# Optimization experiments

Hardware: AMD Instinct MI355X
Metric: run time of the kernel (lower is better)

The kernel has to match this reference:

```python
import jax, jax.numpy as jnp
import numpy as np

B, D, U, HU = 2048, 1024, 1024, 256

def _ln(x, eps=1e-3):
    # Keras LayerNormalization(center=False, scale=False), default epsilon=1e-3
    m = jnp.mean(x, axis=-1, keepdims=True)
    v = jnp.var(x, axis=-1, keepdims=True)
    return (x - m) * jax.lax.rsqrt(v + eps)

def setup_inputs() -> dict:
    key = jax.random.key(0)
    ks = jax.random.split(key, 17)
    s = 0.02
    return {
        "inputs": jax.random.normal(ks[0], (B, D), jnp.float32),
        "main_h": 0.1 * jax.random.normal(ks[1], (B, U), jnp.float32),
        "main_c": 0.1 * jax.random.normal(ks[2], (B, U), jnp.float32),
        "hyper_h": 0.1 * jax.random.normal(ks[3], (B, HU), jnp.float32),
        "hyper_c": 0.1 * jax.random.normal(ks[4], (B, HU), jnp.float32),
        "kernel": s * jax.random.normal(ks[5], (D, 4 * U), jnp.float32),
        "recurrent_kernel": s * jax.random.normal(ks[6], (U, 4 * U), jnp.float32),
        "bias": jnp.zeros((4 * U,), jnp.float32),
        "hyper_kernel": s * jax.random.normal(ks[7], (D + U, 4 * HU), jnp.float32),
        "hyper_rec_kernel": s * jax.random.normal(ks[8], (HU, 4 * HU), jnp.float32),
        "hyper_bias": jnp.zeros((4 * HU,), jnp.float32),
        "dx_w": s * jax.random.normal(ks[9], (HU, 4 * U), jnp.float32),
        "dx_b": s * jax.random.normal(ks[10], (4 * U,), jnp.float32),
        "dh_w": s * jax.random.normal(ks[11], (HU, 4 * U), jnp.float32),
        "dh_b": s * jax.random.normal(ks[12], (4 * U,), jnp.float32),
        "db_w": s * jax.random.normal(ks[13], (HU, 4 * U), jnp.float32),
        "db_b": s * jax.random.normal(ks[14], (4 * U,), jnp.float32),
    }

def reference(inputs, main_h, main_c, hyper_h, hyper_c,
              kernel, recurrent_kernel, bias,
              hyper_kernel, hyper_rec_kernel, hyper_bias,
              dx_w, dx_b, dh_w, dh_b, db_w, db_b):
    # --- hyper LSTMCell (Keras gate order i, f, g, o) ---
    hx = jnp.concatenate([inputs, main_h], axis=-1)          # [B, D+U]
    z = hx @ hyper_kernel + hyper_h @ hyper_rec_kernel + hyper_bias  # [B, 4*HU]
    hi, hf, hg, ho = jnp.split(z, 4, axis=-1)
    hyper_c_new = jax.nn.sigmoid(hf) * hyper_c + jax.nn.sigmoid(hi) * jnp.tanh(hg)
    hyper_out = jax.nn.sigmoid(ho) * jnp.tanh(hyper_c_new)  # = hyper_h_new

    # --- hypernet gate scalings ---
    d_x = hyper_out @ dx_w + dx_b                            # [B, 4*U]
    d_h = hyper_out @ dh_w + dh_b
    d_b = hyper_out @ db_w + db_b

    # --- main LSTM gates with hyper modulation + LayerNorm ---
    proj_x = inputs @ kernel + bias                          # [B, 4*U]
    proj_h = main_h @ recurrent_kernel                       # [B, 4*U]
    gates = _ln(d_x * proj_x + d_h * proj_h + d_b)
    i, f, g, o = jnp.split(gates, 4, axis=-1)
    main_c_new = jax.nn.sigmoid(f) * main_c + jax.nn.sigmoid(i) * jnp.tanh(g)
    main_h_new = jax.nn.sigmoid(o) * jnp.tanh(_ln(main_c_new))
    return (main_h_new, main_c_new, hyper_out, hyper_c_new)
```

## Files before the change

### kernel.cpp

```cpp
#include <hip/hip_runtime.h>
#include <cstdint>

typedef unsigned short u16;
typedef _Float16 half8 __attribute__((ext_vector_type(8)));
typedef float floatx4 __attribute__((ext_vector_type(4)));

#define BB 2048
#define UU 1024
#define HUx 256
#define O_H  0
#define O_C  (BB*UU)
#define O_HO (2*BB*UU)
#define O_HC (2*BB*UU + BB*HUx)
#define MFMAH __builtin_amdgcn_mfma_f32_16x16x32_f16

#define LBAR() do { \
    asm volatile("s_waitcnt lgkmcnt(0)\n\ts_barrier" ::: "memory"); \
    __builtin_amdgcn_sched_barrier(0); \
} while (0)

__device__ __forceinline__ float bf2f(u16 u) {
    union { uint32_t i; float f; } v; v.i = ((uint32_t)u) << 16; return v.f;
}
__device__ __forceinline__ u16 f2bf(float f) {
    union { float f; uint32_t i; } v; v.f = f;
    uint32_t r = v.i + 0x7fffu + ((v.i >> 16) & 1u);
    return (u16)(r >> 16);
}
__device__ __forceinline__ u16 f2h(float f) {
    _Float16 h = (_Float16)f; u16 u; __builtin_memcpy(&u, &h, 2); return u;
}
__device__ __forceinline__ float sigf(float x) { return 1.f / (1.f + expf(-x)); }
__device__ __forceinline__ float ldmix(const void* p, size_t i, int isbf) {
    return isbf ? bf2f(((const u16*)p)[i]) : ((const float*)p)[i];
}
__device__ __forceinline__ u16 ld2h(const void* p, size_t i, int isbf) {
    return f2h(ldmix(p, i, isbf));
}

__device__ __forceinline__ void stage_sync(u16* lds, const u16* src, int row0, int ldK,
                                           int k0, int rows, int tid) {
    for (int v = tid; v < rows * 4; v += 256) {
        int r = v >> 2, c = (v & 3) * 8;
        half8 d = *(const half8*)(src + (size_t)(row0 + r) * ldK + k0 + c);
        *(half8*)&lds[r * 40 + c] = d;
    }
}

__device__ __forceinline__ void ld128(half8 r[2], const u16* src, int row0, int ldK,
                                      int k0, int tid) {
    #pragma unroll
    for (int i = 0; i < 2; i++) {
        int v = tid + 256 * i;
        r[i] = *(const half8*)(src + (size_t)(row0 + (v >> 2)) * ldK + k0 + (v & 3) * 8);
    }
}
__device__ __forceinline__ void ld64(half8& r, const u16* src, int row0, int ldK,
                                     int k0, int tid) {
    r = *(const half8*)(src + (size_t)(row0 + (tid >> 2)) * ldK + k0 + (tid & 3) * 8);
}
__device__ __forceinline__ void wr128(u16* lds, const half8 r[2], int tid) {
    #pragma unroll
    for (int i = 0; i < 2; i++) {
        int v = tid + 256 * i;
        *(half8*)&lds[(v >> 2) * 40 + (v & 3) * 8] = r[i];
    }
}
__device__ __forceinline__ void wr64(u16* lds, half8 r, int tid) {
    *(half8*)&lds[(tid >> 2) * 40 + (tid & 3) * 8] = r;
}

__global__ void detect_dtype(const u16* __restrict__ raw, int* __restrict__ flag) {
    u16 u = raw[2 * threadIdx.x];
    int e = (u >> 7) & 0xFF;
    unsigned long long m = __ballot(e >= 100 && e <= 134);
    if (threadIdx.x == 0) *flag = (__popcll(m) >= 32) ? 1 : 0;
}

__global__ void cvt_all(const void* __restrict__ xs, const void* __restrict__ ms,
                        const void* __restrict__ hs, u16* __restrict__ xh,
                        u16* __restrict__ mh, u16* __restrict__ hh, const int* __restrict__ flag) {
    int i = blockIdx.x * 256 + threadIdx.x;
    int isbf = *flag;
    const void* src; u16* dst; int t;
    if (i < 262144)      { src = xs; dst = xh; t = i; }
    else if (i < 524288) { src = ms; dst = mh; t = i - 262144; }
    else                 { src = hs; dst = hh; t = i - 524288; }
    #pragma unroll
    for (int j = 0; j < 8; j++)
        dst[(size_t)t * 8 + j] = ld2h(src, (size_t)t * 8 + j, isbf);
}

__global__ void transpose_cvt(const void* __restrict__ in, u16* __restrict__ out,
                              int R, int C, int ostride, int ocol,
                              const int* __restrict__ flag) {
    __shared__ u16 th[32][33];
    int isbf = *flag;
    int c0 = blockIdx.x * 32, r0 = blockIdx.y * 32;
    int tx = threadIdx.x, ty = threadIdx.y;
    #pragma unroll
    for (int i = 0; i < 32; i += 8)
        th[ty + i][tx] = ld2h(in, (size_t)(r0 + ty + i) * C + c0 + tx, isbf);
    __syncthreads();
    #pragma unroll
    for (int i = 0; i < 32; i += 8)
        out[(size_t)(c0 + ty + i) * ostride + ocol + r0 + tx] = th[tx][ty + i];
}

__global__ void transpose_z(const void* __restrict__ i0, const void* __restrict__ i1,
                            const void* __restrict__ i2, u16* __restrict__ o0,
                            u16* __restrict__ o1, u16* __restrict__ o2,
                            int R, int C, int ostride, const int* __restrict__ flag) {
    __shared__ u16 th[32][33];
    const void* in = (blockIdx.z == 0) ? i0 : (blockIdx.z == 1) ? i1 : i2;
    u16* out = (blockIdx.z == 0) ? o0 : (blockIdx.z == 1) ? o1 : o2;
    int isbf = *flag;
    int c0 = blockIdx.x * 32, r0 = blockIdx.y * 32;
    int tx = threadIdx.x, ty = threadIdx.y;
    #pragma unroll
    for (int i = 0; i < 32; i += 8)
        th[ty + i][tx] = ld2h(in, (size_t)(r0 + ty + i) * C + c0 + tx, isbf);
    __syncthreads();
    #pragma unroll
    for (int i = 0; i < 32; i += 8)
        out[(size_t)(c0 + ty + i) * ostride + r0 + tx] = th[tx][ty + i];
}

__device__ __forceinline__ void gh_load(half8 pA[2], half8& pB,
                                        const u16* xh, const u16* mh, const u16* hh,
                                        const u16* BT, int bm, int bn, int s, int tid) {
    const u16* Ap; int ldA, kA;
    if (s < 32)      { Ap = xh; ldA = 1024; kA = s * 32; }
    else if (s < 64) { Ap = mh; ldA = 1024; kA = (s - 32) * 32; }
    else             { Ap = hh; ldA = 256;  kA = (s - 64) * 32; }
    ld128(pA, Ap, bm, ldA, kA, tid);
    ld64(pB, BT, bn, 2304, s * 32, tid);
}

__global__ __launch_bounds__(256) void gemm_hyper(const u16* __restrict__ xh,
                                                  const u16* __restrict__ mh,
                                                  const u16* __restrict__ hh,
                                                  const u16* __restrict__ BT,
                                                  float* __restrict__ z) {
    __shared__ __align__(16) u16 sA[128 * 40];
    __shared__ __align__(16) u16 sB[64 * 40];
    int tid = threadIdx.x, lane = tid & 63, wave = tid >> 6;
    int wm = (wave & 1) * 64, wn = (wave >> 1) * 32;
    int bm = blockIdx.y * 128, bn = blockIdx.x * 64;
    int s0 = blockIdx.z * 36, s1 = s0 + 36;
    floatx4 acc[4][2] = {};
    int mr = lane & 15, kq = (lane >> 4) * 8;

    half8 pA[2]; half8 pB;
    gh_load(pA, pB, xh, mh, hh, BT, bm, bn, s0, tid);
    wr128(sA, pA, tid); wr64(sB, pB, tid);
    gh_load(pA, pB, xh, mh, hh, BT, bm, bn, s0 + 1, tid);
    LBAR();

    #pragma unroll 1
    for (int s = s0; s < s1; s++) {
        half8 a[4], b[2];
        #pragma unroll
        for (int t = 0; t < 4; t++) a[t] = *(const half8*)&sA[(wm + t * 16 + mr) * 40 + kq];
        #pragma unroll
        for (int t = 0; t < 2; t++) b[t] = *(const half8*)&sB[(wn + t * 16 + mr) * 40 + kq];
        #pragma unroll
        for (int tm = 0; tm < 4; tm++)
            #pragma unroll
            for (int tn = 0; tn < 2; tn++)
                acc[tm][tn] = MFMAH(a[tm], b[tn], acc[tm][tn], 0, 0, 0);
        LBAR();
        if (s < s1 - 1) {
            wr128(sA, pA, tid); wr64(sB, pB, tid);
            if (s < s1 - 2)
                gh_load(pA, pB, xh, mh, hh, BT, bm, bn, s + 2, tid);
            LBAR();
        }
    }

    float* zp = z + (size_t)blockIdx.z * 2048 * 1024;
    #pragma unroll
    for (int tm = 0; tm < 4; tm++)
        #pragma unroll
        for (int tn = 0; tn < 2; tn++) {
            int col = bn + wn + tn * 16 + (lane & 15);
            #pragma unroll
            for (int rr = 0; rr < 4; rr++) {
                int row = bm + wm + tm * 16 + (lane >> 4) * 4 + rr;
                zp[(size_t)row * 1024 + col] = acc[tm][tn][rr];
            }
        }
}

__global__ void hyper_cell(const float* __restrict__ z, const void* __restrict__ hyper_c,
                           const void* __restrict__ hyper_bias, void* __restrict__ out,
                           u16* __restrict__ ho16, const int* __restrict__ flag) {
    int isbf = *flag;
    int t = blockIdx.x * 256 + threadIdx.x;
    int k = t & 255;
    const float* zr  = z + (size_t)(t >> 8) * 1024;
    const float* zr2 = zr + (size_t)2048 * 1024;
    float hi = zr[k]       + zr2[k]       + ldmix(hyper_bias, k, isbf);
    float hf = zr[k + 256] + zr2[k + 256] + ldmix(hyper_bias, k + 256, isbf);
    float hg = zr[k + 512] + zr2[k + 512] + ldmix(hyper_bias, k + 512, isbf);
    float ho = zr[k + 768] + zr2[k + 768] + ldmix(hyper_bias, k + 768, isbf);
    float c  = ldmix(hyper_c, t, isbf);
    float cn = sigf(hf) * c + sigf(hi) * tanhf(hg);
    float hout = sigf(ho) * tanhf(cn);
    ho16[t] = f2h(hout);
    if (isbf) {
        ((u16*)out)[O_HO + t] = f2bf(hout);
        ((u16*)out)[O_HC + t] = f2bf(cn);
    } else {
        ((float*)out)[O_HO + t] = hout;
        ((float*)out)[O_HC + t] = cn;
    }
}

__global__ __launch_bounds__(256, 2) void mega_fused(
    const u16* __restrict__ xh, const u16* __restrict__ mh, const u16* __restrict__ ho16,
    const u16* __restrict__ kT, const u16* __restrict__ rkT,
    const u16* __restrict__ dxT, const u16* __restrict__ dhT, const u16* __restrict__ dbT,
    const void* __restrict__ bias, const void* __restrict__ dx_b,
    const void* __restrict__ dh_b, const void* __restrict__ db_b,
    u16* __restrict__ gp, const int* __restrict__ flag) {
    __shared__ __align__(16) u16 sA1[128 * 40];
    __shared__ __align__(16) u16 sA2[128 * 40];
    __shared__ __align__(16) u16 sB1[64 * 40];
    __shared__ __align__(16) u16 sB2[64 * 40];
    __shared__ __align__(16) u16 sB3[64 * 40];
    int isbf = *flag;
    int tid = threadIdx.x, lane = tid & 63, wave = tid >> 6;
    int wm = (wave & 1) * 64, wn = (wave >> 1) * 32;
    int bm = blockIdx.y * 128, bn = blockIdx.x * 64;
    floatx4 apx[4][2] = {}, aph[4][2] = {}, adx[4][2] = {}, adh[4][2] = {}, adb[4][2] = {};
    int mr = lane & 15, kq = (lane >> 4) * 8;

    half8 nA1[2], nA2[2], nB1a, nB2a, nB3a;

    ld128(nA1, xh,  bm, 1024, 0, tid);
    ld128(nA2, mh,  bm, 1024, 0, tid);
    ld64(nB1a, kT,  bn, 1024, 0, tid);
    ld64(nB2a, rkT, bn, 1024, 0, tid);
    wr128(sA1, nA1, tid); wr128(sA2, nA2, tid);
    wr64(sB1, nB1a, tid); wr64(sB2, nB2a, tid);
    ld128(nA1, xh,  bm, 1024, 32, tid);
    ld128(nA2, mh,  bm, 1024, 32, tid);
    ld64(nB1a, kT,  bn, 1024, 32, tid);
    ld64(nB2a, rkT, bn, 1024, 32, tid);
    LBAR();

    #pragma unroll 1
    for (int k0 = 0; k0 < 1024; k0 += 32) {
        half8 ax[4], am[4], bk[2], br[2];
        #pragma unroll
        for (int t = 0; t < 4; t++) {
            int ra = (wm + t * 16 + mr) * 40 + kq;
            ax[t] = *(const half8*)&sA1[ra];
            am[t] = *(const half8*)&sA2[ra];
        }
        #pragma unroll
        for (int t = 0; t < 2; t++) {
            int rb = (wn + t * 16 + mr) * 40 + kq;
            bk[t] = *(const half8*)&sB1[rb];
            br[t] = *(const half8*)&sB2[rb];
        }
        #pragma unroll
        for (int tm = 0; tm < 4; tm++)
            #pragma unroll
            for (int tn = 0; tn < 2; tn++) {
                apx[tm][tn] = MFMAH(ax[tm], bk[tn], apx[tm][tn], 0, 0, 0);
                aph[tm][tn] = MFMAH(am[tm], br[tn], aph[tm][tn], 0, 0, 0);
            }
        LBAR();
        if (k0 < 1024 - 32) {
            wr128(sA1, nA1, tid); wr128(sA2, nA2, tid);
            wr64(sB1, nB1a, tid); wr64(sB2, nB2a, tid);
            if (k0 < 1024 - 64) {
                ld128(nA1, xh,  bm, 1024, k0 + 64, tid);
                ld128(nA2, mh,  bm, 1024, k0 + 64, tid);
                ld64(nB1a, kT,  bn, 1024, k0 + 64, tid);
                ld64(nB2a, rkT, bn, 1024, k0 + 64, tid);
            } else {
                ld128(nA1, ho16, bm, 256, 0, tid);
                ld64(nB1a, dxT,  bn, 256, 0, tid);
                ld64(nB2a, dhT,  bn, 256, 0, tid);
                ld64(nB3a, dbT,  bn, 256, 0, tid);
            }
            LBAR();
        }
    }

    wr128(sA1, nA1, tid);
    wr64(sB1, nB1a, tid); wr64(sB2, nB2a, tid); wr64(sB3, nB3a, tid);
    ld128(nA1, ho16, bm, 256, 32, tid);
    ld64(nB1a, dxT,  bn, 256, 32, tid);
    ld64(nB2a, dhT,  bn, 256, 32, tid);
    ld64(nB3a, dbT,  bn, 256, 32, tid);
    LBAR();

    #pragma unroll 1
    for (int k0 = 0; k0 < 256; k0 += 32) {
        half8 a[4], bx[2], bh[2], bb[2];
        #pragma unroll
        for (int t = 0; t < 4; t++) {
            int ra = (wm + t * 16 + mr) * 40 + kq;
            a[t] = *(const half8*)&sA1[ra];
        }
        #pragma unroll
        for (int t = 0; t < 2; t++) {
            int rb = (wn + t * 16 + mr) * 40 + kq;
            bx[t] = *(const half8*)&sB1[rb];
            bh[t] = *(const half8*)&sB2[rb];
            bb[t] = *(const half8*)&sB3[rb];
        }
        #pragma unroll
        for (int tm = 0; tm < 4; tm++)
            #pragma unroll
            for (int tn = 0; tn < 2; tn++) {
                adx[tm][tn] = MFMAH(a[tm], bx[tn], adx[tm][tn], 0, 0, 0);
                adh[tm][tn] = MFMAH(a[tm], bh[tn], adh[tm][tn], 0, 0, 0);
                adb[tm][tn] = MFMAH(a[tm], bb[tn], adb[tm][tn], 0, 0, 0);
            }
        LBAR();
        if (k0 < 256 - 32) {
            wr128(sA1, nA1, tid);
            wr64(sB1, nB1a, tid); wr64(sB2, nB2a, tid); wr64(sB3, nB3a, tid);
            if (k0 < 256 - 64) {
                ld128(nA1, ho16, bm, 256, k0 + 64, tid);
                ld64(nB1a, dxT,  bn, 256, k0 + 64, tid);
                ld64(nB2a, dhT,  bn, 256, k0 + 64, tid);
                ld64(nB3a, dbT,  bn, 256, k0 + 64, tid);
            }
            LBAR();
        }
    }

    #pragma unroll
    for (int tn = 0; tn < 2; tn++) {
        int col = bn + wn + tn * 16 + (lane & 15);
        float bv  = ldmix(bias, col, isbf);
        float dxb = ldmix(dx_b, col, isbf);
        float dhb = ldmix(dh_b, col, isbf);
        float dbb = ldmix(db_b, col, isbf);
        #pragma unroll
        for (int tm = 0; tm < 4; tm++) {
            #pragma unroll
            for (int rr = 0; rr < 4; rr++) {
                int row = bm + wm + tm * 16 + (lane >> 4) * 4 + rr;
                float px = apx[tm][tn][rr] + bv;
                float ph = aph[tm][tn][rr];
                float dx = adx[tm][tn][rr] + dxb;
                float dh = adh[tm][tn][rr] + dhb;
                float db = adb[tm][tn][rr] + dbb;
                gp[(size_t)row * 4096 + col] = f2h(dx * px + dh * ph + db);
            }
        }
    }
}

__device__ __forceinline__ void block_reduce2(float& a, float& b, float* red) {
    #pragma unroll
    for (int o = 32; o > 0; o >>= 1) {
        a += __shfl_down(a, o, 64);
        b += __shfl_down(b, o, 64);
    }
    int lane = threadIdx.x & 63, w = threadIdx.x >> 6;
    if (lane == 0) { red[w] = a; red[4 + w] = b; }
    __syncthreads();
    a = red[0] + red[1] + red[2] + red[3];
    b = red[4] + red[5] + red[6] + red[7];
    __syncthreads();
}

__global__ __launch_bounds__(256) void ln_main(const u16* __restrict__ gp,
                                               const void* __restrict__ main_c,
                                               void* __restrict__ out,
                                               const int* __restrict__ flag) {
    __shared__ float sPre[4096];
    __shared__ float sC[1024];
    __shared__ float red[8];
    int isbf = *flag;
    int b = blockIdx.x, tid = threadIdx.x;
    const u16* g = gp + (size_t)b * 4096;
    float s = 0.f, q = 0.f;
    for (int j0 = tid * 8; j0 < 4096; j0 += 2048) {
        half8 v = *(const half8*)(g + j0);
        #pragma unroll
        for (int e = 0; e < 8; e++) {
            float f = (float)v[e];
            sPre[j0 + e] = f; s += f; q += f * f;
        }
    }
    block_reduce2(s, q, red);
    float mean = s * (1.f / 4096.f);
    float var = q * (1.f / 4096.f) - mean * mean;
    float rs = rsqrtf(var + 1e-3f);
    float s2 = 0.f, q2 = 0.f;
    for (int u = tid; u < 1024; u += 256) {
        float gi = (sPre[u] - mean) * rs;
        float gf = (sPre[u + 1024] - mean) * rs;
        float gg = (sPre[u + 2048] - mean) * rs;
        float c = ldmix(main_c, (size_t)b * 1024 + u, isbf);
        float cn = sigf(gf) * c + sigf(gi) * tanhf(gg);
        sC[u] = cn;
        if (isbf) ((u16*)out)[O_C + (size_t)b * 1024 + u] = f2bf(cn);
        else      ((float*)out)[O_C + (size_t)b * 1024 + u] = cn;
        s2 += cn; q2 += cn * cn;
    }
    block_reduce2(s2, q2, red);
    float m2 = s2 * (1.f / 1024.f);
    float v2 = q2 * (1.f / 1024.f) - m2 * m2;
    float rs2 = rsqrtf(v2 + 1e-3f);
    for (int u = tid; u < 1024; u += 256) {
        float go = (sPre[u + 3072] - mean) * rs;
        float hn = sigf(go) * tanhf((sC[u] - m2) * rs2);
        if (isbf) ((u16*)out)[O_H + (size_t)b * 1024 + u] = f2bf(hn);
        else      ((float*)out)[O_H + (size_t)b * 1024 + u] = hn;
    }
}

extern "C" void kernel_launch(void* const* d_in, const int* in_sizes, int n_in,
                              void* d_out, int out_size, void* d_ws, size_t ws_size,
                              hipStream_t stream) {
    (void)in_sizes; (void)n_in; (void)out_size; (void)ws_size;
    const void* inputs   = d_in[0];
    const void* main_h   = d_in[1];
    const void* main_c   = d_in[2];
    const void* hyper_h  = d_in[3];
    const void* hyper_c  = d_in[4];
    const void* kernel_w = d_in[5];
    const void* rec_w    = d_in[6];
    const void* bias     = d_in[7];
    const void* hyper_k  = d_in[8];
    const void* hyper_rk = d_in[9];
    const void* hyper_b  = d_in[10];
    const void* dx_w = d_in[11];
    const void* dx_b = d_in[12];
    const void* dh_w = d_in[13];
    const void* dh_b = d_in[14];
    const void* db_w = d_in[15];
    const void* db_b = d_in[16];
    char* ws = (char*)d_ws;
    const size_t MB = 1024 * 1024;

    int* flag = (int*)ws;
    size_t off = 256;
    u16* xh  = (u16*)(ws + off); off += 4 * MB;
    u16* mh  = (u16*)(ws + off); off += 4 * MB;
    u16* hh  = (u16*)(ws + off); off += 1 * MB;
    u16* ho  = (u16*)(ws + off); off += 1 * MB;
    u16* kT  = (u16*)(ws + off); off += 8 * MB;
    u16* rkT = (u16*)(ws + off); off += 8 * MB;
    u16* dxT = (u16*)(ws + off); off += 2 * MB;
    u16* dhT = (u16*)(ws + off); off += 2 * MB;
    u16* dbT = (u16*)(ws + off); off += 2 * MB;
    u16* BTh = (u16*)(ws + off); off += (size_t)1024 * 2304 * 2;
    float* zbuf = (float*)(ws + off); off += 16 * MB;
    u16* gp    = (u16*)(ws + off); off += 16 * MB;

    detect_dtype<<<1, 64, 0, stream>>>((const u16*)inputs, flag);
    cvt_all<<<2304, 256, 0, stream>>>(inputs, main_h, hyper_h, xh, mh, hh, flag);

    dim3 tblk(32, 8);
    transpose_cvt<<<dim3(32, 64), tblk, 0, stream>>>(hyper_k, BTh, 2048, 1024, 2304, 0, flag);
    transpose_cvt<<<dim3(32, 8),  tblk, 0, stream>>>(hyper_rk, BTh, 256, 1024, 2304, 2048, flag);
    transpose_z<<<dim3(128, 32, 2), tblk, 0, stream>>>(kernel_w, rec_w, rec_w,
                                                       kT, rkT, rkT, 1024, 4096, 1024, flag);
    transpose_z<<<dim3(128, 8, 3), tblk, 0, stream>>>(dx_w, dh_w, db_w,
                                                      dxT, dhT, dbT, 256, 4096, 256, flag);

    gemm_hyper<<<dim3(16, 16, 2), 256, 0, stream>>>(xh, mh, hh, BTh, zbuf);
    hyper_cell<<<2048, 256, 0, stream>>>(zbuf, hyper_c, hyper_b, d_out, ho, flag);
    mega_fused<<<dim3(64, 16), 256, 0, stream>>>(xh, mh, ho, kT, rkT, dxT, dhT, dbT,
                                                 bias, dx_b, dh_b, db_b, gp, flag);
    ln_main<<<2048, 256, 0, stream>>>(gp, main_c, d_out, flag);
}
```

Before: 299.4 us.

## Load A operands directly from global into registers, bypassing LDS

The A-matrix tiles (inputs, main_h, hyper_out) are now loaded by each wave straight from global memory into MFMA operand registers, double-buffered across unrolled K steps, instead of being staged through shared memory. This removes the LDS write/read traffic and LDS space for A, which may allow more occupancy. In exchange, A rows are re-fetched from global/L2 by both N-direction waves, and the per-lane 16-byte loads are less coalesced. Register pressure also rises from holding four extra half8 sets.

```diff
diff --git a/kernel.cpp b/kernel.cpp
--- a/kernel.cpp
+++ b/kernel.cpp
@@ -38,15 +38,6 @@
     return f2h(ldmix(p, i, isbf));
 }
 
-__device__ __forceinline__ void stage_sync(u16* lds, const u16* src, int row0, int ldK,
-                                           int k0, int rows, int tid) {
-    for (int v = tid; v < rows * 4; v += 256) {
-        int r = v >> 2, c = (v & 3) * 8;
-        half8 d = *(const half8*)(src + (size_t)(row0 + r) * ldK + k0 + c);
-        *(half8*)&lds[r * 40 + c] = d;
-    }
-}
-
 __device__ __forceinline__ void ld128(half8 r[2], const u16* src, int row0, int ldK,
                                       int k0, int tid) {
     #pragma unroll
@@ -68,6 +59,13 @@
 }
 __device__ __forceinline__ void wr64(u16* lds, half8 r, int tid) {
     *(half8*)&lds[(tid >> 2) * 40 + (tid & 3) * 8] = r;
+}
+
+__device__ __forceinline__ void ldA4(half8 r[4], const u16* src, int row0, int ldK,
+                                     int k0, int mr, int kq) {
+    #pragma unroll
+    for (int t = 0; t < 4; t++)
+        r[t] = *(const half8*)(src + (size_t)(row0 + t * 16 + mr) * ldK + k0 + kq);
 }
 
 __global__ void detect_dtype(const u16* __restrict__ raw, int* __restrict__ flag) {
@@ -224,8 +222,6 @@
     const void* __restrict__ bias, const void* __restrict__ dx_b,
     const void* __restrict__ dh_b, const void* __restrict__ db_b,
     u16* __restrict__ gp, const int* __restrict__ flag) {
-    __shared__ __align__(16) u16 sA1[128 * 40];
-    __shared__ __align__(16) u16 sA2[128 * 40];
     __shared__ __align__(16) u16 sB1[64 * 40];
     __shared__ __align__(16) u16 sB2[64 * 40];
     __shared__ __align__(16) u16 sB3[64 * 40];
@@ -235,106 +231,106 @@
     int bm = blockIdx.y * 128, bn = blockIdx.x * 64;
     floatx4 apx[4][2] = {}, aph[4][2] = {}, adx[4][2] = {}, adh[4][2] = {}, adb[4][2] = {};
     int mr = lane & 15, kq = (lane >> 4) * 8;
-
-    half8 nA1[2], nA2[2], nB1a, nB2a, nB3a;
-
-    ld128(nA1, xh,  bm, 1024, 0, tid);
-    ld128(nA2, mh,  bm, 1024, 0, tid);
+    int arow = bm + wm;
+
+    half8 nB1a, nB2a, nB3a;
+    half8 axA[4], amA[4], axB[4], amB[4];
+
     ld64(nB1a, kT,  bn, 1024, 0, tid);
     ld64(nB2a, rkT, bn, 1024, 0, tid);
-    wr128(sA1, nA1, tid); wr128(sA2, nA2, tid);
     wr64(sB1, nB1a, tid); wr64(sB2, nB2a, tid);
-    ld128(nA1, xh,  bm, 1024, 32, tid);
-    ld128(nA2, mh,  bm, 1024, 32, tid);
     ld64(nB1a, kT,  bn, 1024, 32, tid);
     ld64(nB2a, rkT, bn, 1024, 32, tid);
+    ldA4(axA, xh, arow, 1024, 0, mr, kq);
+    ldA4(amA, mh, arow, 1024, 0, mr, kq);
     LBAR();
 
+    #define P1_STEP(AXC, AMC, AXN, AMN, K0)                                    \
+    do {                                                                       \
+        if ((K0) + 32 < 1024) {                                                \
+            ldA4(AXN, xh, arow, 1024, (K0) + 32, mr, kq);                      \
+            ldA4(AMN, mh, arow, 1024, (K0) + 32, mr, kq);                      \
+        }                                                                      \
+        half8 bk[2], br[2];                                                    \
+        _Pragma("unroll")                                                      \
+        for (int t = 0; t < 2; t++) {                                          \
+            int rb = (wn + t * 16 + mr) * 40 + kq;                             \
+            bk[t] = *(const half8*)&sB1[rb];                                   \
+            br[t] = *(const half8*)&sB2[rb];                                   \
+        }                                                                      \
+        _Pragma("unroll")                                                      \
+        for (int tm = 0; tm < 4; tm++)                                         \
+            _Pragma("unroll")                                                  \
+            for (int tn = 0; tn < 2; tn++) {                                   \
+                apx[tm][tn] = MFMAH((AXC)[tm], bk[tn], apx[tm][tn], 0, 0, 0);  \
+                aph[tm][tn] = MFMAH((AMC)[tm], br[tn], aph[tm][tn], 0, 0, 0);  \
+            }                                                                  \
+        LBAR();                                                                \
+        if ((K0) < 992) {                                                      \
+            wr64(sB1, nB1a, tid); wr64(sB2, nB2a, tid);                        \
+            if ((K0) < 960) {                                                  \
+                ld64(nB1a, kT,  bn, 1024, (K0) + 64, tid);                     \
+                ld64(nB2a, rkT, bn, 1024, (K0) + 64, tid);                     \
+            } else {                                                           \
+                ld64(nB1a, dxT, bn, 256, 0, tid);                              \
+                ld64(nB2a, dhT, bn, 256, 0, tid);                              \
+                ld64(nB3a, dbT, bn, 256, 0, tid);                              \
+            }                                                                  \
+            LBAR();                                                            \
+        }                                                                      \
+    } while (0)
+
     #pragma unroll 1
-    for (int k0 = 0; k0 < 1024; k0 += 32) {
-        half8 ax[4], am[4], bk[2], br[2];
-        #pragma unroll
-        for (int t = 0; t < 4; t++) {
-            int ra = (wm + t * 16 + mr) * 40 + kq;
-            ax[t] = *(const half8*)&sA1[ra];
-            am[t] = *(const half8*)&sA2[ra];
-        }
-        #pragma unroll
-        for (int t = 0; t < 2; t++) {
-            int rb = (wn + t * 16 + mr) * 40 + kq;
-            bk[t] = *(const half8*)&sB1[rb];
-            br[t] = *(const half8*)&sB2[rb];
-        }
-        #pragma unroll
-        for (int tm = 0; tm < 4; tm++)
-            #pragma unroll
-            for (int tn = 0; tn < 2; tn++) {
-                apx[tm][tn] = MFMAH(ax[tm], bk[tn], apx[tm][tn], 0, 0, 0);
-                aph[tm][tn] = MFMAH(am[tm], br[tn], aph[tm][tn], 0, 0, 0);
-            }
-        LBAR();
-        if (k0 < 1024 - 32) {
-            wr128(sA1, nA1, tid); wr128(sA2, nA2, tid);
-            wr64(sB1, nB1a, tid); wr64(sB2, nB2a, tid);
-            if (k0 < 1024 - 64) {
-                ld128(nA1, xh,  bm, 1024, k0 + 64, tid);
-                ld128(nA2, mh,  bm, 1024, k0 + 64, tid);
-                ld64(nB1a, kT,  bn, 1024, k0 + 64, tid);
-                ld64(nB2a, rkT, bn, 1024, k0 + 64, tid);
-            } else {
-                ld128(nA1, ho16, bm, 256, 0, tid);
-                ld64(nB1a, dxT,  bn, 256, 0, tid);
-                ld64(nB2a, dhT,  bn, 256, 0, tid);
-                ld64(nB3a, dbT,  bn, 256, 0, tid);
-            }
-            LBAR();
-        }
-    }
-
-    wr128(sA1, nA1, tid);
+    for (int k0 = 0; k0 < 1024; k0 += 64) {
+        P1_STEP(axA, amA, axB, amB, k0);
+        P1_STEP(axB, amB, axA, amA, k0 + 32);
+    }
+    #undef P1_STEP
+
     wr64(sB1, nB1a, tid); wr64(sB2, nB2a, tid); wr64(sB3, nB3a, tid);
-    ld128(nA1, ho16, bm, 256, 32, tid);
-    ld64(nB1a, dxT,  bn, 256, 32, tid);
-    ld64(nB2a, dhT,  bn, 256, 32, tid);
-    ld64(nB3a, dbT,  bn, 256, 32, tid);
+    ld64(nB1a, dxT, bn, 256, 32, tid);
+    ld64(nB2a, dhT, bn, 256, 32, tid);
+    ld64(nB3a, dbT, bn, 256, 32, tid);
+    ldA4(axA, ho16, arow, 256, 0, mr, kq);
     LBAR();
 
+    #define P2_STEP(AC, AN, K0)                                                \
+    do {                                                                       \
+        if ((K0) + 32 < 256) ldA4(AN, ho16, arow, 256, (K0) + 32, mr, kq);     \
+        half8 bx[2], bh[2], bb[2];                                             \
+        _Pragma("unroll")                                                      \
+        for (int t = 0; t < 2; t++) {                                          \
+            int rb = (wn + t * 16 + mr) * 40 + kq;                             \
+            bx[t] = *(const half8*)&sB1[rb];                                   \
+            bh[t] = *(const half8*)&sB2[rb];                                   \
+            bb[t] = *(const half8*)&sB3[rb];                                   \
+        }                                                                      \
+        _Pragma("unroll")                                                      \
+        for (int tm = 0; tm < 4; tm++)                                         \
+            _Pragma("unroll")                                                  \
+            for (int tn = 0; tn < 2; tn++) {                                   \
+                adx[tm][tn] = MFMAH((AC)[tm], bx[tn], adx[tm][tn], 0, 0, 0);   \
+                adh[tm][tn] = MFMAH((AC)[tm], bh[tn], adh[tm][tn], 0, 0, 0);   \
+                adb[tm][tn] = MFMAH((AC)[tm], bb[tn], adb[tm][tn], 0, 0, 0);   \
+            }                                                                  \
+        LBAR();                                                                \
+        if ((K0) < 224) {                                                      \
+            wr64(sB1, nB1a, tid); wr64(sB2, nB2a, tid); wr64(sB3, nB3a, tid);  \
+            if ((K0) < 192) {                                                  \
+                ld64(nB1a, dxT, bn, 256, (K0) + 64, tid);                      \
+                ld64(nB2a, dhT, bn, 256, (K0) + 64, tid);                      \
+                ld64(nB3a, dbT, bn, 256, (K0) + 64, tid);                      \
+            }                                                                  \
+            LBAR();                                                            \
+        }                                                                      \
+    } while (0)
+
     #pragma unroll 1
-    for (int k0 = 0; k0 < 256; k0 += 32) {
-        half8 a[4], bx[2], bh[2], bb[2];
-        #pragma unroll
-        for (int t = 0; t < 4; t++) {
-            int ra = (wm + t * 16 + mr) * 40 + kq;
-            a[t] = *(const half8*)&sA1[ra];
-        }
-        #pragma unroll
-        for (int t = 0; t < 2; t++) {
-            int rb = (wn + t * 16 + mr) * 40 + kq;
-            bx[t] = *(const half8*)&sB1[rb];
-            bh[t] = *(const half8*)&sB2[rb];
-            bb[t] = *(const half8*)&sB3[rb];
-        }
-        #pragma unroll
-        for (int tm = 0; tm < 4; tm++)
-            #pragma unroll
-            for (int tn = 0; tn < 2; tn++) {
-                adx[tm][tn] = MFMAH(a[tm], bx[tn], adx[tm][tn], 0, 0, 0);
-                adh[tm][tn] = MFMAH(a[tm], bh[tn], adh[tm][tn], 0, 0, 0);
-                adb[tm][tn] = MFMAH(a[tm], bb[tn], adb[tm][tn], 0, 0, 0);
-            }
-        LBAR();
-        if (k0 < 256 - 32) {
-            wr128(sA1, nA1, tid);
-            wr64(sB1, nB1a, tid); wr64(sB2, nB2a, tid); wr64(sB3, nB3a, tid);
-            if (k0 < 256 - 64) {
-                ld128(nA1, ho16, bm, 256, k0 + 64, tid);
-                ld64(nB1a, dxT,  bn, 256, k0 + 64, tid);
-                ld64(nB2a, dhT,  bn, 256, k0 + 64, tid);
-                ld64(nB3a, dbT,  bn, 256, k0 + 64, tid);
-            }
-            LBAR();
-        }
-    }
+    for (int k0 = 0; k0 < 256; k0 += 64) {
+        P2_STEP(axA, axB, k0);
+        P2_STEP(axB, axA, k0 + 32);
+    }
+    #undef P2_STEP
 
     #pragma unroll
     for (int tn = 0; tn < 2; tn++) {
```

After: 365.6 us. +22.1%, slower.
